# Performance work log

Measured on AMD Instinct MI355X. Metric: run time of the kernel, lower is better.

Reference implementation:

```python
import jax, jax.numpy as jnp
import numpy as np

DECAY = 0.99
EPS = 1e-05
COMMIT = 0.25


def setup_inputs() -> dict:
    key = jax.random.key(0)
    k1, k2 = jax.random.split(key)
    dim, n_embed = 256, 8192
    z = jax.random.normal(k1, (32, 32, 32, dim), dtype=jnp.float32)
    embed = jax.random.normal(k2, (dim, n_embed), dtype=jnp.float32)
    cluster_size = jnp.zeros((n_embed,), dtype=jnp.float32)
    embed_avg = embed  # torch init: embed_avg = embed.clone()
    return {"z": z, "embed": embed, "cluster_size": cluster_size, "embed_avg": embed_avg}


def reference(z, embed, cluster_size, embed_avg):
    dim, n_embed = embed.shape
    flatten = z.reshape(-1, dim)                       # [N, D]
    # squared L2 distance to each code: ||f||^2 - 2 f.E + ||E||^2
    dist = ((flatten ** 2).sum(1, keepdims=True)
            - 2.0 * flatten @ embed
            + (embed ** 2).sum(0, keepdims=True))      # [N, K]
    ind = jnp.argmin(dist, axis=1)                     # [N]
    quantize = jnp.take(embed.T, ind, axis=0).reshape(z.shape)
    embed_ind = ind.reshape(z.shape[:-1])

    # EMA codebook update (training mode), via segment_sum instead of a dense one-hot
    counts = jax.ops.segment_sum(jnp.ones_like(ind, dtype=flatten.dtype), ind,
                                 num_segments=n_embed)          # [K]
    embed_sum = jax.ops.segment_sum(flatten, ind,
                                    num_segments=n_embed).T     # [D, K]
    cluster_size_new = cluster_size * DECAY + (1.0 - DECAY) * counts
    embed_avg_new = embed_avg * DECAY + (1.0 - DECAY) * embed_sum
    n = cluster_size_new.sum()
    cs = (cluster_size_new + EPS) / (n + n_embed * EPS) * n
    embed_new = embed_avg_new / cs[None, :]

    diff = COMMIT * jnp.mean((jax.lax.stop_gradient(quantize) - z) ** 2)
    quantize_st = z + jax.lax.stop_gradient(quantize - z)  # straight-through
    return quantize_st, diff, embed_ind, embed_new
```

## Files before the change

### kernel.cpp

```cpp
#include <hip/hip_runtime.h>
#include <hip/hip_bf16.h>

#define D 256
#define K 8192
#define NTOT 32768
#define BM 128
#define BN2 128
#define BD 32
#define CSPLIT 4
#define CT_PER (K / CSPLIT / BN2)

typedef __bf16 bf16x8 __attribute__((ext_vector_type(8)));
typedef float f32x4 __attribute__((ext_vector_type(4)));

__device__ __forceinline__ void gl_lds16(const void* g, void* l) {
    __builtin_amdgcn_global_load_lds(
        (__attribute__((address_space(1))) void*)(g),
        (__attribute__((address_space(3))) void*)(l), 16, 0, 0);
}

__device__ __forceinline__ unsigned int enc_f32(float f) {
    unsigned int u = __float_as_uint(f);
    return (u & 0x80000000u) ? ~u : (u | 0x80000000u);
}

__device__ __forceinline__ unsigned short f2bfu(float x) {
    __hip_bfloat16 h = __float2bfloat16(x);
    return __builtin_bit_cast(unsigned short, h);
}
__device__ __forceinline__ float bfu2f(unsigned short u) {
    return __bfloat162float(__builtin_bit_cast(__hip_bfloat16, u));
}

__global__ __launch_bounds__(256)
void conv_F(const float* __restrict__ z, unsigned short* __restrict__ Fhi,
            unsigned short* __restrict__ Flo) {
    int i4 = blockIdx.x * 256 + threadIdx.x;
    float4 v = ((const float4*)z)[i4];
    ushort4 h, l;
    h.x = f2bfu(v.x); l.x = f2bfu(v.x - bfu2f(h.x));
    h.y = f2bfu(v.y); l.y = f2bfu(v.y - bfu2f(h.y));
    h.z = f2bfu(v.z); l.z = f2bfu(v.z - bfu2f(h.z));
    h.w = f2bfu(v.w); l.w = f2bfu(v.w - bfu2f(h.w));
    ((ushort4*)Fhi)[i4] = h;
    ((ushort4*)Flo)[i4] = l;
}

__global__ __launch_bounds__(256)
void conv_E(const float* __restrict__ E, const float* __restrict__ cs_in,
            unsigned short* __restrict__ EhiT, unsigned short* __restrict__ EloT,
            float* __restrict__ ET, float* __restrict__ enorm,
            float* __restrict__ nsum) {
    __shared__ float tile[64][65];
    int tid = threadIdx.x;
    int k0 = blockIdx.x * 64, d0 = blockIdx.y * 64;

    if (blockIdx.y == 0 && tid < 64) {
        float s = cs_in[k0 + tid];
#pragma unroll
        for (int off = 32; off; off >>= 1) s += __shfl_down(s, off);
        if (tid == 0) atomicAdd(nsum, s);
    }

#pragma unroll
    for (int it = 0; it < 16; ++it) {
        int idx = it * 256 + tid;
        int dr = idx >> 6, kc = idx & 63;
        tile[kc][dr] = E[(d0 + dr) * K + k0 + kc];
    }
    __syncthreads();
#pragma unroll
    for (int it = 0; it < 16; ++it) {
        int idx = it * 256 + tid;
        int kr = idx >> 6, dc = idx & 63;
        float v = tile[kr][dc];
        unsigned short h = f2bfu(v);
        int o = (k0 + kr) * D + d0 + dc;
        EhiT[o] = h;
        EloT[o] = f2bfu(v - bfu2f(h));
        ET[o] = v;
        float ss = v * v;
#pragma unroll
        for (int off = 32; off; off >>= 1) ss += __shfl_down(ss, off);
        if ((tid & 63) == 0) atomicAdd(&enorm[k0 + kr], ss);
    }
}

__global__ __launch_bounds__(256)
void mfma_dist_argmin(const unsigned short* __restrict__ Fhi,
                      const unsigned short* __restrict__ Flo,
                      const unsigned short* __restrict__ EhiT,
                      const unsigned short* __restrict__ EloT,
                      const float* __restrict__ enorm,
                      unsigned long long* __restrict__ bestpack) {
    __shared__ unsigned short Ah[BM * BD], Al[BM * BD], Bh[BN2 * BD], Bl[BN2 * BD];

    const int tid = threadIdx.x;
    const int wave = tid >> 6;
    const int lane = tid & 63;
    const int qd = lane >> 4;
    const int ln = lane & 15;
    const int wm = (wave >> 1) * 64;
    const int wn = (wave & 1) * 64;
    const int n0 = blockIdx.x * BM;
    const int c0 = blockIdx.y * (K / CSPLIT);
    const int r_ = tid >> 2;
    const int s_sw = (tid & 3) ^ ((tid >> 3) & 3);
    const int csw = (qd ^ ((ln >> 1) & 3)) * 8;

    float bestv[16];
    int besti[16];
#pragma unroll
    for (int i = 0; i < 16; ++i) { bestv[i] = 3.402823466e38f; besti[i] = 0; }

    for (int ct = 0; ct < CT_PER; ++ct) {
        const int cb = c0 + ct * BN2;
        f32x4 acc[4][4];
#pragma unroll
        for (int mi = 0; mi < 4; ++mi)
#pragma unroll
            for (int ni = 0; ni < 4; ++ni) acc[mi][ni] = (f32x4){0.f, 0.f, 0.f, 0.f};

        for (int d0 = 0; d0 < D; d0 += BD) {
            __syncthreads();
#pragma unroll
            for (int it = 0; it < 2; ++it) {
                const int ga = (n0 + it * 64 + r_) * D + d0 + s_sw * 8;
                const int gb = (cb + it * 64 + r_) * D + d0 + s_sw * 8;
                const int lo = it * 2048 + wave * 512;
                gl_lds16(Fhi + ga, &Ah[lo]);
                gl_lds16(Flo + ga, &Al[lo]);
                gl_lds16(EhiT + gb, &Bh[lo]);
                gl_lds16(EloT + gb, &Bl[lo]);
            }
            __syncthreads();

            bf16x8 ah[4], al[4], bh[4], bl[4];
#pragma unroll
            for (int mi = 0; mi < 4; ++mi) {
                int off = (wm + mi * 16 + ln) * BD + csw;
                ah[mi] = *(const bf16x8*)&Ah[off];
                al[mi] = *(const bf16x8*)&Al[off];
            }
#pragma unroll
            for (int ni = 0; ni < 4; ++ni) {
                int off = (wn + ni * 16 + ln) * BD + csw;
                bh[ni] = *(const bf16x8*)&Bh[off];
                bl[ni] = *(const bf16x8*)&Bl[off];
            }
#pragma unroll
            for (int mi = 0; mi < 4; ++mi)
#pragma unroll
                for (int ni = 0; ni < 4; ++ni)
                    acc[mi][ni] = __builtin_amdgcn_mfma_f32_16x16x32_bf16(
                        ah[mi], bh[ni], acc[mi][ni], 0, 0, 0);
#pragma unroll
            for (int mi = 0; mi < 4; ++mi)
#pragma unroll
                for (int ni = 0; ni < 4; ++ni)
                    acc[mi][ni] = __builtin_amdgcn_mfma_f32_16x16x32_bf16(
                        ah[mi], bl[ni], acc[mi][ni], 0, 0, 0);
#pragma unroll
            for (int mi = 0; mi < 4; ++mi)
#pragma unroll
                for (int ni = 0; ni < 4; ++ni)
                    acc[mi][ni] = __builtin_amdgcn_mfma_f32_16x16x32_bf16(
                        al[mi], bh[ni], acc[mi][ni], 0, 0, 0);
        }

        float en[4];
#pragma unroll
        for (int ni = 0; ni < 4; ++ni) en[ni] = enorm[cb + wn + ni * 16 + ln];
#pragma unroll
        for (int ni = 0; ni < 4; ++ni) {
            int k = cb + wn + ni * 16 + ln;
#pragma unroll
            for (int mi = 0; mi < 4; ++mi) {
                f32x4 a = acc[mi][ni];
#pragma unroll
                for (int r = 0; r < 4; ++r) {
                    float dist = en[ni] - 2.0f * a[r];
                    int bi = mi * 4 + r;
                    if (dist < bestv[bi]) { bestv[bi] = dist; besti[bi] = k; }
                }
            }
        }
    }

#pragma unroll
    for (int mi = 0; mi < 4; ++mi) {
#pragma unroll
        for (int r = 0; r < 4; ++r) {
            int bi = mi * 4 + r;
            float v = bestv[bi];
            int ix = besti[bi];
#pragma unroll
            for (int off = 1; off < 16; off <<= 1) {
                float v2 = __shfl_xor(v, off);
                int i2 = __shfl_xor(ix, off);
                if (v2 < v || (v2 == v && i2 < ix)) { v = v2; ix = i2; }
            }
            if (ln == 0) {
                int m = n0 + wm + mi * 16 + qd * 4 + r;
                unsigned long long pack =
                    ((unsigned long long)enc_f32(v) << 32) | (unsigned int)ix;
                atomicMin(&bestpack[m], pack);
            }
        }
    }
}

#define ROWS_PER_BLOCK 16
__global__ __launch_bounds__(256)
void assign_apply(const float* __restrict__ z,
                  const float* __restrict__ ET,
                  const unsigned long long* __restrict__ bestpack,
                  float* __restrict__ out_q, float* __restrict__ out_ind,
                  float* __restrict__ counts, float* __restrict__ esumT,
                  float* __restrict__ diffpart) {
    const int tx = threadIdx.x;
    const int rbase = blockIdx.x * ROWS_PER_BLOCK;
    float part = 0.f;
    for (int r = 0; r < ROWS_PER_BLOCK; ++r) {
        int n = rbase + r;
        unsigned long long p = bestpack[n];
        int idx = (int)(p & 0xFFFFFFFFull);
        float f = z[n * D + tx];
        float q = ET[idx * D + tx];
        out_q[n * D + tx] = q;
        float dd = q - f;
        part += dd * dd;
        atomicAdd(&esumT[idx * D + tx], f);
        if (tx == 0) {
            atomicAdd(&counts[idx], 1.0f);
            out_ind[n] = (float)idx;
        }
    }
#pragma unroll
    for (int off = 32; off; off >>= 1) part += __shfl_down(part, off);
    __shared__ float wsum[4];
    if ((tx & 63) == 0) wsum[tx >> 6] = part;
    __syncthreads();
    if (tx == 0) diffpart[blockIdx.x] = wsum[0] + wsum[1] + wsum[2] + wsum[3];
}

__global__ __launch_bounds__(256)
void finalize(const float* __restrict__ eavg, const float* __restrict__ esumT,
              const float* __restrict__ cs_in, const float* __restrict__ counts,
              const float* __restrict__ nsum, const float* __restrict__ diffpart,
              float* __restrict__ out_enew, float* __restrict__ out_diff) {
    const int tid = threadIdx.x;
    if (blockIdx.x == 0) {
        float p = 0.f;
#pragma unroll
        for (int j = 0; j < 8; ++j) p += diffpart[tid + 256 * j];
#pragma unroll
        for (int off = 32; off; off >>= 1) p += __shfl_down(p, off);
        __shared__ float sred[4];
        if ((tid & 63) == 0) sred[tid >> 6] = p;
        __syncthreads();
        if (tid == 0)
            *out_diff = (sred[0] + sred[1] + sred[2] + sred[3]) * (0.25f / 8388608.0f);
    }
    const int idx = blockIdx.x * 256 + tid;
    const float nv = 0.99f * nsum[0] + 0.01f * 32768.0f;
    const int k = idx & (K - 1);
    const int d = idx >> 13;
    const float csn_k = 0.99f * cs_in[k] + 0.01f * counts[k];
    const float avg_new = 0.99f * eavg[idx] + 0.01f * esumT[k * D + d];
    const float cs = (csn_k + 1e-5f) / (nv + 0.08192f) * nv;
    out_enew[idx] = avg_new / cs;
}

extern "C" void kernel_launch(void* const* d_in, const int* in_sizes, int n_in,
                              void* d_out, int out_size, void* d_ws, size_t ws_size,
                              hipStream_t stream) {
    const float* z = (const float*)d_in[0];
    const float* embed = (const float*)d_in[1];
    const float* cs_in = (const float*)d_in[2];
    const float* eavg = (const float*)d_in[3];

    float* out = (float*)d_out;
    float* out_q = out;
    float* out_diff = out + 8388608;
    float* out_ind = out + 8388609;
    float* out_enew = out + 8421377;

    char* ws = (char*)d_ws;
    unsigned long long* bestpack = (unsigned long long*)ws;
    float* counts = (float*)(ws + 262144);
    float* nsum = (float*)(ws + 294912);
    float* enorm = (float*)(ws + 295168);
    float* esumT = (float*)(ws + 327936);
    unsigned short* Fhi = (unsigned short*)(ws + 8716544);
    unsigned short* Flo = (unsigned short*)(ws + 25493760);
    unsigned short* EhiT = (unsigned short*)(ws + 42270976);
    unsigned short* EloT = (unsigned short*)(ws + 46465280);
    float* ET = (float*)(ws + 50659584);
    float* diffpart = (float*)(ws + 8716544);

    hipMemsetAsync(bestpack, 0xFF, 262144, stream);
    hipMemsetAsync(ws + 262144, 0, 8454400, stream);

    conv_F<<<NTOT * D / 4 / 256, 256, 0, stream>>>(z, Fhi, Flo);
    conv_E<<<dim3(K / 64, D / 64), 256, 0, stream>>>(embed, cs_in, EhiT, EloT, ET,
                                                     enorm, nsum);
    mfma_dist_argmin<<<dim3(NTOT / BM, CSPLIT), 256, 0, stream>>>(Fhi, Flo, EhiT, EloT,
                                                                  enorm, bestpack);
    assign_apply<<<NTOT / ROWS_PER_BLOCK, 256, 0, stream>>>(z, ET, bestpack, out_q,
                                                            out_ind, counts, esumT,
                                                            diffpart);
    finalize<<<(D * K) / 256, 256, 0, stream>>>(eavg, esumT, cs_in, counts, nsum,
                                                diffpart, out_enew, out_diff);
}
```

Before: 584.6 us.

## Keep the full feature tile resident in LDS and use 512-thread blocks

The distance/argmin kernel now loads the block's whole 128x256 hi/lo bf16 feature tile into LDS once, with an XOR swizzle, instead of reloading feature slices for every codebook tile. Only codebook slices are streamed per d-step. Blocks grow to 8 waves with a 4x2 wave layout covering 64x32 each, and the codebook split drops from 4 to 2. This removes repeated global-to-LDS traffic for the features, but uses about 136KB of LDS per block, which limits occupancy to one block per CU, and halves the grid size.

```diff
diff --git a/kernel.cpp b/kernel.cpp
--- a/kernel.cpp
+++ b/kernel.cpp
@@ -7,7 +7,7 @@
 #define BM 128
 #define BN2 128
 #define BD 32
-#define CSPLIT 4
+#define CSPLIT 2
 #define CT_PER (K / CSPLIT / BN2)
 
 typedef __bf16 bf16x8 __attribute__((ext_vector_type(8)));
@@ -86,27 +86,43 @@
     }
 }
 
-__global__ __launch_bounds__(256)
+__global__ __launch_bounds__(512)
 void mfma_dist_argmin(const unsigned short* __restrict__ Fhi,
                       const unsigned short* __restrict__ Flo,
                       const unsigned short* __restrict__ EhiT,
                       const unsigned short* __restrict__ EloT,
                       const float* __restrict__ enorm,
                       unsigned long long* __restrict__ bestpack) {
-    __shared__ unsigned short Ah[BM * BD], Al[BM * BD], Bh[BN2 * BD], Bl[BN2 * BD];
+    __shared__ unsigned short Ahr[BM * D];
+    __shared__ unsigned short Alr[BM * D];
+    __shared__ unsigned short Bh[BN2 * BD];
+    __shared__ unsigned short Bl[BN2 * BD];
 
     const int tid = threadIdx.x;
     const int wave = tid >> 6;
     const int lane = tid & 63;
     const int qd = lane >> 4;
     const int ln = lane & 15;
-    const int wm = (wave >> 1) * 64;
-    const int wn = (wave & 1) * 64;
+    const int wm = (wave >> 2) * 64;
+    const int wn = (wave & 3) * 32;
     const int n0 = blockIdx.x * BM;
     const int c0 = blockIdx.y * (K / CSPLIT);
-    const int r_ = tid >> 2;
-    const int s_sw = (tid & 3) ^ ((tid >> 3) & 3);
     const int csw = (qd ^ ((ln >> 1) & 3)) * 8;
+
+#pragma unroll
+    for (int i = 0; i < 8; ++i) {
+        const int row = i * 16 + (tid >> 5);
+        const int pw = (tid & 31) >> 2;
+        const int pc = tid & 3;
+        const int gw = pw ^ (row & 1);
+        const int gc = pc ^ ((row >> 1) & 3);
+        const int ga = (n0 + row) * D + gw * 32 + gc * 8;
+        gl_lds16(Fhi + ga, &Ahr[i * 4096 + wave * 512]);
+        gl_lds16(Flo + ga, &Alr[i * 4096 + wave * 512]);
+    }
+
+    const int brow = tid >> 2;
+    const int bsw = (tid & 3) ^ ((tid >> 3) & 3);
 
     float bestv[16];
     int besti[16];
@@ -115,65 +131,63 @@
 
     for (int ct = 0; ct < CT_PER; ++ct) {
         const int cb = c0 + ct * BN2;
-        f32x4 acc[4][4];
+        f32x4 acc[4][2];
 #pragma unroll
         for (int mi = 0; mi < 4; ++mi)
 #pragma unroll
-            for (int ni = 0; ni < 4; ++ni) acc[mi][ni] = (f32x4){0.f, 0.f, 0.f, 0.f};
+            for (int ni = 0; ni < 2; ++ni) acc[mi][ni] = (f32x4){0.f, 0.f, 0.f, 0.f};
 
         for (int d0 = 0; d0 < D; d0 += BD) {
             __syncthreads();
-#pragma unroll
-            for (int it = 0; it < 2; ++it) {
-                const int ga = (n0 + it * 64 + r_) * D + d0 + s_sw * 8;
-                const int gb = (cb + it * 64 + r_) * D + d0 + s_sw * 8;
-                const int lo = it * 2048 + wave * 512;
-                gl_lds16(Fhi + ga, &Ah[lo]);
-                gl_lds16(Flo + ga, &Al[lo]);
-                gl_lds16(EhiT + gb, &Bh[lo]);
-                gl_lds16(EloT + gb, &Bl[lo]);
+            {
+                const int gb = (cb + brow) * D + d0 + bsw * 8;
+                gl_lds16(EhiT + gb, &Bh[wave * 512]);
+                gl_lds16(EloT + gb, &Bl[wave * 512]);
             }
             __syncthreads();
 
-            bf16x8 ah[4], al[4], bh[4], bl[4];
+            const int w = d0 >> 5;
+            bf16x8 ah[4], al[4], bh[2], bl[2];
 #pragma unroll
             for (int mi = 0; mi < 4; ++mi) {
-                int off = (wm + mi * 16 + ln) * BD + csw;
-                ah[mi] = *(const bf16x8*)&Ah[off];
-                al[mi] = *(const bf16x8*)&Al[off];
-            }
-#pragma unroll
-            for (int ni = 0; ni < 4; ++ni) {
-                int off = (wn + ni * 16 + ln) * BD + csw;
-                bh[ni] = *(const bf16x8*)&Bh[off];
-                bl[ni] = *(const bf16x8*)&Bl[off];
-            }
+                const int arow = wm + mi * 16 + ln;
+                const int aoff = arow * D + ((w ^ (arow & 1)) << 5) + csw;
+                ah[mi] = *(const bf16x8*)&Ahr[aoff];
+                al[mi] = *(const bf16x8*)&Alr[aoff];
+            }
+#pragma unroll
+            for (int ni = 0; ni < 2; ++ni) {
+                const int boff = (wn + ni * 16 + ln) * BD + csw;
+                bh[ni] = *(const bf16x8*)&Bh[boff];
+                bl[ni] = *(const bf16x8*)&Bl[boff];
+            }
+
 #pragma unroll
             for (int mi = 0; mi < 4; ++mi)
 #pragma unroll
-                for (int ni = 0; ni < 4; ++ni)
+                for (int ni = 0; ni < 2; ++ni)
                     acc[mi][ni] = __builtin_amdgcn_mfma_f32_16x16x32_bf16(
                         ah[mi], bh[ni], acc[mi][ni], 0, 0, 0);
 #pragma unroll
             for (int mi = 0; mi < 4; ++mi)
 #pragma unroll
-                for (int ni = 0; ni < 4; ++ni)
+                for (int ni = 0; ni < 2; ++ni)
                     acc[mi][ni] = __builtin_amdgcn_mfma_f32_16x16x32_bf16(
                         ah[mi], bl[ni], acc[mi][ni], 0, 0, 0);
 #pragma unroll
             for (int mi = 0; mi < 4; ++mi)
 #pragma unroll
-                for (int ni = 0; ni < 4; ++ni)
+                for (int ni = 0; ni < 2; ++ni)
                     acc[mi][ni] = __builtin_amdgcn_mfma_f32_16x16x32_bf16(
                         al[mi], bh[ni], acc[mi][ni], 0, 0, 0);
         }
 
-        float en[4];
-#pragma unroll
-        for (int ni = 0; ni < 4; ++ni) en[ni] = enorm[cb + wn + ni * 16 + ln];
-#pragma unroll
-        for (int ni = 0; ni < 4; ++ni) {
-            int k = cb + wn + ni * 16 + ln;
+        float en[2];
+#pragma unroll
+        for (int ni = 0; ni < 2; ++ni) en[ni] = enorm[cb + wn + ni * 16 + ln];
+#pragma unroll
+        for (int ni = 0; ni < 2; ++ni) {
+            const int k = cb + wn + ni * 16 + ln;
 #pragma unroll
             for (int mi = 0; mi < 4; ++mi) {
                 f32x4 a = acc[mi][ni];
@@ -305,7 +319,7 @@
     conv_F<<<NTOT * D / 4 / 256, 256, 0, stream>>>(z, Fhi, Flo);
     conv_E<<<dim3(K / 64, D / 64), 256, 0, stream>>>(embed, cs_in, EhiT, EloT, ET,
                                                      enorm, nsum);
-    mfma_dist_argmin<<<dim3(NTOT / BM, CSPLIT), 256, 0, stream>>>(Fhi, Flo, EhiT, EloT,
+    mfma_dist_argmin<<<dim3(NTOT / BM, CSPLIT), 512, 0, stream>>>(Fhi, Flo, EhiT, EloT,
                                                                   enorm, bestpack);
     assign_apply<<<NTOT / ROWS_PER_BLOCK, 256, 0, stream>>>(z, ET, bestpack, out_q,
                                                             out_ind, counts, esumT,
```

Result: slower. 640.8 us (+9.6%).
